# Performance work log

Hardware: AMD Instinct MI355X
Metric: run time of the kernel (lower is better)

## Reference

```python
import jax, jax.numpy as jnp
import numpy as np

D_MODEL = 768
NUM_HEADS = 12
D_HEAD = D_MODEL // NUM_HEADS


def setup_inputs() -> dict:
    key = jax.random.key(0)
    ks = jax.random.split(key, 11)
    B, S = 1, 4096
    s = 1.0 / np.sqrt(D_MODEL)
    inp = {
        'q': jax.random.normal(ks[0], (B, S, D_MODEL), dtype=jnp.float32),
        'k': jax.random.normal(ks[1], (B, S, D_MODEL), dtype=jnp.float32),
        'v': jax.random.normal(ks[2], (B, S, D_MODEL), dtype=jnp.float32),
        'wq': jax.random.normal(ks[3], (D_MODEL, D_MODEL), dtype=jnp.float32) * s,
        'bq': jnp.zeros((D_MODEL,), dtype=jnp.float32),
        'wk': jax.random.normal(ks[4], (D_MODEL, D_MODEL), dtype=jnp.float32) * s,
        'bk': jnp.zeros((D_MODEL,), dtype=jnp.float32),
        'wv': jax.random.normal(ks[5], (D_MODEL, D_MODEL), dtype=jnp.float32) * s,
        'bv': jnp.zeros((D_MODEL,), dtype=jnp.float32),
        'wo': jax.random.normal(ks[6], (D_MODEL, D_MODEL), dtype=jnp.float32) * s,
        'bo': jnp.zeros((D_MODEL,), dtype=jnp.float32),
    }
    return inp


def reference(q, k, v, wq, bq, wk, bk, wv, bv, wo, bo):
    B, S, _ = q.shape
    # linear projections (torch Linear: x @ W^T + b)
    qh = (q @ wq.T + bq).reshape(B, S, NUM_HEADS, D_HEAD).transpose(0, 2, 1, 3)
    kh = (k @ wk.T + bk).reshape(B, S, NUM_HEADS, D_HEAD).transpose(0, 2, 1, 3)
    vh = (v @ wv.T + bv).reshape(B, S, NUM_HEADS, D_HEAD).transpose(0, 2, 1, 3)
    scores = jnp.einsum('bhqd,bhkd->bhqk', qh, kh) / jnp.sqrt(jnp.float32(D_HEAD))
    causal = jnp.tril(jnp.ones((S, S), dtype=bool))  # [S,S] causal mask
    scores = jnp.where(causal, scores, jnp.finfo(scores.dtype).min)
    attn = jax.nn.softmax(scores, axis=-1)  # dropout omitted (eval mode)
    out = jnp.einsum('bhqk,bhkd->bhqd', attn, vh)
    out = out.transpose(0, 2, 1, 3).reshape(B, S, D_MODEL)
    return out @ wo.T + bo
```

## Files before the change

kernel.cpp:

```cpp
#include <hip/hip_runtime.h>
#include <stdint.h>

typedef __attribute__((ext_vector_type(8))) short short8;
typedef __attribute__((ext_vector_type(2))) float float2v;
typedef __attribute__((ext_vector_type(4))) float float4v;
typedef __attribute__((ext_vector_type(16))) float f32x16;
typedef __attribute__((ext_vector_type(2))) uint32_t uint32x2;
typedef __attribute__((ext_vector_type(4))) uint32_t uint32x4;
typedef __attribute__((ext_vector_type(2))) unsigned int uint2v;

__device__ __forceinline__ uint32_t pkbf(float a, float b) {
  uint32_t r;
  asm("v_cvt_pk_bf16_f32 %0, %1, %2" : "=v"(r) : "v"(a), "v"(b));
  return r;
}

__device__ __forceinline__ float2v pkadd(float2v a, float2v b) {
  float2v d;
  asm("v_pk_add_f32 %0, %1, %2" : "=v"(d) : "v"(a), "v"(b));
  return d;
}

__device__ __forceinline__ float fexp2(float x) {
#if __has_builtin(__builtin_amdgcn_exp2f)
  return __builtin_amdgcn_exp2f(x);
#else
  return exp2f(x);
#endif
}

__device__ __forceinline__ uint2v plswap(uint32_t a, uint32_t b) {
#if __has_builtin(__builtin_amdgcn_permlane32_swap)
  return __builtin_amdgcn_permlane32_swap(a, b, false, false);
#else
  asm("v_permlane32_swap_b32 %0, %1" : "+v"(a), "+v"(b));
  uint2v r;
  r[0] = a;
  r[1] = b;
  return r;
#endif
}

__device__ __forceinline__ void gll16(const unsigned short* g, unsigned short* l) {
  __builtin_amdgcn_global_load_lds(
      (const __attribute__((address_space(1))) void*)g,
      (__attribute__((address_space(3))) void*)l, 16, 0, 0);
}

struct CvtArgs {
  const float* src[7];
  unsigned short* dst[7];
};

__global__ __launch_bounds__(256) void cvt_all(CvtArgs a) {
  const int bid = blockIdx.x;
  int t, off;
  if (bid < 4608) { t = bid / 1536; off = bid - t * 1536; }
  else { const int b2 = bid - 4608; t = 3 + b2 / 288; off = b2 - (t - 3) * 288; }
  const size_t i = (size_t)off * 256 + threadIdx.x;
  const float4v* p = (const float4v*)(a.src[t] + i * 8);
  float4v x = p[0], y = p[1];
  uint32x4 o;
  o[0] = pkbf(x[0], x[1]);
  o[1] = pkbf(x[2], x[3]);
  o[2] = pkbf(y[0], y[1]);
  o[3] = pkbf(y[2], y[3]);
  *(uint32x4*)(a.dst[t] + i * 8) = o;
}

__global__ __launch_bounds__(256) void gemm_qkv(
    const unsigned short* __restrict__ xq, const unsigned short* __restrict__ xk,
    const unsigned short* __restrict__ xv,
    const unsigned short* __restrict__ wqb, const unsigned short* __restrict__ wkb,
    const unsigned short* __restrict__ wvb,
    const float* __restrict__ bq, const float* __restrict__ bk,
    const float* __restrict__ bv,
    unsigned short* __restrict__ Qp, unsigned short* __restrict__ Kp,
    unsigned short* __restrict__ Vt, float qscale)
{
  __shared__ unsigned short As[128 * 64];
  __shared__ unsigned short Ws[128 * 64];
  const int z = blockIdx.z;
  const unsigned short* A = z == 0 ? xq : z == 1 ? xk : xv;
  const unsigned short* W = z == 0 ? wqb : z == 1 ? wkb : wvb;
  const float* bias = z == 0 ? bq : z == 1 ? bk : bv;
  const int M = 4096, N = 768, K = 768;
  const int tid = threadIdx.x, wave = tid >> 6, lane = tid & 63;
  const int g = lane >> 4, l16 = lane & 15;
  const int sw = l16 & 7;
  const int m0 = blockIdx.x * 128, n0 = blockIdx.y * 128;
  const int wn = (wave >> 1) * 64, wm = (wave & 1) * 64;
  const int srow0 = wave * 32 + (lane >> 3);
  const int skg = lane & 7;

  float4v acc[4][4] = {};

  for (int k0 = 0; k0 < K; k0 += 64) {
    if (k0) __syncthreads();
    #pragma unroll
    for (int c = 0; c < 4; ++c) {
      const int row = srow0 + c * 8;
      const int kg = skg ^ (row & 7);
      gll16(A + (size_t)(m0 + row) * K + k0 + kg * 8, &As[(wave * 32 + c * 8) * 64]);
      gll16(W + (size_t)(n0 + row) * K + k0 + kg * 8, &Ws[(wave * 32 + c * 8) * 64]);
    }
    __syncthreads();
    #pragma unroll
    for (int kk = 0; kk < 2; ++kk) {
      const int kg = ((kk * 4 + g) ^ sw) * 8;
      short8 xf[4], wf[4];
      #pragma unroll
      for (int t = 0; t < 4; ++t) {
        xf[t] = *(const short8*)&As[(wm + t * 16 + l16) * 64 + kg];
        wf[t] = *(const short8*)&Ws[(wn + t * 16 + l16) * 64 + kg];
      }
      if (z < 2) {
        #pragma unroll
        for (int i = 0; i < 4; ++i)
          #pragma unroll
          for (int j = 0; j < 4; ++j)
            acc[i][j] = __builtin_amdgcn_mfma_f32_16x16x32_bf16(wf[i], xf[j], acc[i][j], 0, 0, 0);
      } else {
        #pragma unroll
        for (int i = 0; i < 4; ++i)
          #pragma unroll
          for (int j = 0; j < 4; ++j)
            acc[i][j] = __builtin_amdgcn_mfma_f32_16x16x32_bf16(xf[i], wf[j], acc[i][j], 0, 0, 0);
      }
    }
  }

  if (z < 2) {
    unsigned short* O = z == 0 ? Qp : Kp;
    const float osc = z == 0 ? qscale : 1.0f;
    #pragma unroll
    for (int i = 0; i < 4; ++i) {
      const int nb = n0 + wn + i * 16 + 4 * g;
      const float4v bb = *(const float4v*)&bias[nb];
      #pragma unroll
      for (int j = 0; j < 4; ++j) {
        const int m = m0 + wm + j * 16 + l16;
        uint32x2 pk;
        pk[0] = pkbf((acc[i][j][0] + bb[0]) * osc, (acc[i][j][1] + bb[1]) * osc);
        pk[1] = pkbf((acc[i][j][2] + bb[2]) * osc, (acc[i][j][3] + bb[3]) * osc);
        *(uint32x2*)(O + (size_t)m * N + nb) = pk;
      }
    }
  } else {
    #pragma unroll
    for (int j = 0; j < 4; ++j) {
      const int n = n0 + wn + j * 16 + l16;
      const float bb = bias[n];
      #pragma unroll
      for (int i = 0; i < 4; ++i) {
        const int mb = m0 + wm + i * 16 + 4 * g;
        uint32x2 pk;
        pk[0] = pkbf(acc[i][j][0] + bb, acc[i][j][1] + bb);
        pk[1] = pkbf(acc[i][j][2] + bb, acc[i][j][3] + bb);
        *(uint32x2*)(Vt + (size_t)n * M + mb) = pk;
      }
    }
  }
}

__global__ __launch_bounds__(256, 4) void flash_part(
    const unsigned short* __restrict__ Qp,
    const unsigned short* __restrict__ Kp,
    const unsigned short* __restrict__ Vt,
    unsigned short* __restrict__ Opart,
    float* __restrict__ lpart)
{
  __shared__ unsigned short lds_k[2][64 * 64];
  __shared__ unsigned short lds_v[2][64 * 64];
  const int S = 4096, DM = 768;

  const int gid = blockIdx.x;
  const int h = gid % 12;
  const int e = 79 - gid / 12;
  int t, c;
  if (e < 8)       { t = e;                c = 0; }
  else if (e < 24) { t = 8 + (e - 8) / 2;  c = (e - 8) % 2; }
  else if (e < 48) { t = 16 + (e - 24) / 3; c = (e - 24) % 3; }
  else             { t = 24 + (e - 48) / 4; c = (e - 48) % 4; }
  const int kb0 = c * 16;
  const int kbe = min(kb0 + 16, 2 * t + 2);

  const int tid = threadIdx.x, wave = tid >> 6, lane = tid & 63;
  const int l31 = lane & 31, hi = lane >> 5, sw7 = lane & 7;
  const int qbase = t * 128 + wave * 32;
  const int qrow = qbase + l31;

  short8 qf[4];
  {
    const unsigned short* qp = Qp + (size_t)qrow * DM + h * 64 + hi * 8;
    qf[0] = *(const short8*)(qp);
    qf[1] = *(const short8*)(qp + 16);
    qf[2] = *(const short8*)(qp + 32);
    qf[3] = *(const short8*)(qp + 48);
  }

  f32x16 o0 = {}, o1 = {};
  float2v lsA = {0.f, 0.f}, lsB = {0.f, 0.f};

  const int strow = wave * 16 + (lane >> 3);
  const int skg = lane & 7;

  #pragma unroll
  for (int cc = 0; cc < 2; ++cc) {
    const int row = strow + cc * 8;
    const int kg = skg ^ (row & 7);
    gll16(Kp + (size_t)(kb0 * 64 + row) * DM + h * 64 + kg * 8,
          &lds_k[0][(wave * 16 + cc * 8) * 64]);
    gll16(Vt + (size_t)(h * 64 + row) * S + kb0 * 64 + kg * 8,
          &lds_v[0][(wave * 16 + cc * 8) * 64]);
  }
  __syncthreads();

  for (int kb = kb0; kb < kbe; ++kb) {
    const int cur = kb & 1;
    if (kb + 1 < kbe) {
      const int nb = cur ^ 1;
      #pragma unroll
      for (int cc = 0; cc < 2; ++cc) {
        const int row = strow + cc * 8;
        const int kg = skg ^ (row & 7);
        gll16(Kp + (size_t)((kb + 1) * 64 + row) * DM + h * 64 + kg * 8,
              &lds_k[nb][(wave * 16 + cc * 8) * 64]);
        gll16(Vt + (size_t)(h * 64 + row) * S + (kb + 1) * 64 + kg * 8,
              &lds_v[nb][(wave * 16 + cc * 8) * 64]);
      }
    }
    const unsigned short* kc = lds_k[cur];
    const unsigned short* vc = lds_v[cur];

    f32x16 s0 = {}, s1 = {};
    __builtin_amdgcn_s_setprio(1);
    #pragma unroll
    for (int d4 = 0; d4 < 4; ++d4) {
      const int cg = ((2 * d4 + hi) ^ sw7) * 8;
      short8 ka = *(const short8*)&kc[l31 * 64 + cg];
      short8 kb2 = *(const short8*)&kc[(32 + l31) * 64 + cg];
      s0 = __builtin_amdgcn_mfma_f32_32x32x16_bf16(ka, qf[d4], s0, 0, 0, 0);
      s1 = __builtin_amdgcn_mfma_f32_32x32x16_bf16(kb2, qf[d4], s1, 0, 0, 0);
    }
    __builtin_amdgcn_s_setprio(0);

    const bool diag = (kb + 1) * 64 > qbase;
    short8 pb[4];
    auto sm_pack = [&](const f32x16& sv, int ks, short8* pbp) {
      #pragma unroll
      for (int jh = 0; jh < 2; ++jh) {
        float pe[8];
        if (diag) {
          #pragma unroll
          for (int rr = 0; rr < 8; ++rr) {
            const int key = kb * 64 + ks + (rr & 3) + 8 * (2 * jh + (rr >> 2)) + 4 * hi;
            pe[rr] = fexp2(key <= qrow ? sv[jh * 8 + rr] : -1e30f);
          }
        } else {
          #pragma unroll
          for (int rr = 0; rr < 8; ++rr) pe[rr] = fexp2(sv[jh * 8 + rr]);
        }
        float2v p01 = {pe[0], pe[1]}, p23 = {pe[2], pe[3]};
        float2v p45 = {pe[4], pe[5]}, p67 = {pe[6], pe[7]};
        lsA = pkadd(lsA, pkadd(p01, p45));
        lsB = pkadd(lsB, pkadd(p23, p67));
        const uint32_t x01 = pkbf(pe[0], pe[1]);
        const uint32_t x23 = pkbf(pe[2], pe[3]);
        const uint32_t y01 = pkbf(pe[4], pe[5]);
        const uint32_t y23 = pkbf(pe[6], pe[7]);
        uint2v r01 = plswap(x01, y01);
        uint2v r23 = plswap(x23, y23);
        union { uint32x4 u; short8 s; } w;
        w.u[0] = r01[0];
        w.u[1] = r23[0];
        w.u[2] = r01[1];
        w.u[3] = r23[1];
        pbp[jh] = w.s;
      }
    };
    sm_pack(s0, 0, &pb[0]);
    sm_pack(s1, 32, &pb[2]);

    __builtin_amdgcn_s_setprio(1);
    #pragma unroll
    for (int kk = 0; kk < 4; ++kk) {
      const int cg = ((2 * kk + hi) ^ sw7) * 8;
      short8 va0 = *(const short8*)&vc[l31 * 64 + cg];
      short8 va1 = *(const short8*)&vc[(32 + l31) * 64 + cg];
      o0 = __builtin_amdgcn_mfma_f32_32x32x16_bf16(va0, pb[kk], o0, 0, 0, 0);
      o1 = __builtin_amdgcn_mfma_f32_32x32x16_bf16(va1, pb[kk], o1, 0, 0, 0);
    }
    __builtin_amdgcn_s_setprio(0);

    __syncthreads();
  }

  float L = (lsA[0] + lsA[1]) + (lsB[0] + lsB[1]);
  L += __shfl_xor(L, 32);
  const int slot = (h * 32 + t) * 4 + c;
  if (hi == 0) lpart[slot * 128 + wave * 32 + l31] = L;
  unsigned short* ob = Opart + (size_t)slot * 8192 + (size_t)(wave * 32 + l31) * 64;
  #pragma unroll
  for (int dt = 0; dt < 2; ++dt) {
    const f32x16& oo = dt ? o1 : o0;
    #pragma unroll
    for (int a = 0; a < 4; ++a) {
      uint32x2 ov;
      ov[0] = pkbf(oo[4 * a + 0], oo[4 * a + 1]);
      ov[1] = pkbf(oo[4 * a + 2], oo[4 * a + 3]);
      *(uint32x2*)(ob + dt * 32 + 8 * a + 4 * hi) = ov;
    }
  }
}

__global__ __launch_bounds__(256) void flash_combine(
    const unsigned short* __restrict__ Opart, const float* __restrict__ lpart,
    unsigned short* __restrict__ AO)
{
  const int t = blockIdx.x, h = blockIdx.y;
  const int nc = (2 * t + 17) >> 4;
  const int slot0 = (h * 32 + t) * 4;
  const int tid = threadIdx.x;
  const int qr = tid >> 2, dc = (tid & 3) * 16;
  #pragma unroll
  for (int it = 0; it < 2; ++it) {
    const int ql = it * 64 + qr;
    float acc[16];
    #pragma unroll
    for (int j = 0; j < 16; ++j) acc[j] = 0.0f;
    float lsum = 0.0f;
    for (int cc = 0; cc < nc; ++cc) {
      const int slot = slot0 + cc;
      lsum += lpart[slot * 128 + ql];
      const uint32x4* p = (const uint32x4*)(Opart + (size_t)slot * 8192 + ql * 64 + dc);
      uint32x4 w0 = p[0], w1 = p[1];
      #pragma unroll
      for (int j = 0; j < 4; ++j) {
        union { uint32_t u; float f; } lo, hi;
        lo.u = w0[j] << 16; hi.u = w0[j] & 0xffff0000u;
        acc[2 * j] += lo.f; acc[2 * j + 1] += hi.f;
        lo.u = w1[j] << 16; hi.u = w1[j] & 0xffff0000u;
        acc[8 + 2 * j] += lo.f; acc[8 + 2 * j + 1] += hi.f;
      }
    }
    const float inv = 1.0f / lsum;
    uint32x4 o0, o1;
    #pragma unroll
    for (int j = 0; j < 4; ++j) {
      o0[j] = pkbf(acc[2 * j] * inv, acc[2 * j + 1] * inv);
      o1[j] = pkbf(acc[8 + 2 * j] * inv, acc[8 + 2 * j + 1] * inv);
    }
    unsigned short* dst = AO + (size_t)(t * 128 + ql) * 768 + h * 64 + dc;
    *(uint32x4*)dst = o0;
    *(uint32x4*)(dst + 8) = o1;
  }
}

__global__ __launch_bounds__(256) void gemm_out(
    const unsigned short* __restrict__ A, const unsigned short* __restrict__ W,
    const float* __restrict__ bias, float* __restrict__ Out)
{
  __shared__ unsigned short As[128 * 64];
  __shared__ unsigned short Ws[128 * 64];
  const int N = 768, K = 768;
  const int tid = threadIdx.x, wave = tid >> 6, lane = tid & 63;
  const int g = lane >> 4, l16 = lane & 15;
  const int sw = l16 & 7;
  const int m0 = blockIdx.x * 128, n0 = blockIdx.y * 128;
  const int wn = (wave >> 1) * 64, wm = (wave & 1) * 64;
  const int srow0 = wave * 32 + (lane >> 3);
  const int skg = lane & 7;

  float4v acc[4][4] = {};

  for (int k0 = 0; k0 < K; k0 += 64) {
    if (k0) __syncthreads();
    #pragma unroll
    for (int c = 0; c < 4; ++c) {
      const int row = srow0 + c * 8;
      const int kg = skg ^ (row & 7);
      gll16(A + (size_t)(m0 + row) * K + k0 + kg * 8, &As[(wave * 32 + c * 8) * 64]);
      gll16(W + (size_t)(n0 + row) * K + k0 + kg * 8, &Ws[(wave * 32 + c * 8) * 64]);
    }
    __syncthreads();
    #pragma unroll
    for (int kk = 0; kk < 2; ++kk) {
      const int kg = ((kk * 4 + g) ^ sw) * 8;
      short8 xf[4], wf[4];
      #pragma unroll
      for (int t = 0; t < 4; ++t) {
        xf[t] = *(const short8*)&As[(wm + t * 16 + l16) * 64 + kg];
        wf[t] = *(const short8*)&Ws[(wn + t * 16 + l16) * 64 + kg];
      }
      #pragma unroll
      for (int i = 0; i < 4; ++i)
        #pragma unroll
        for (int j = 0; j < 4; ++j)
          acc[i][j] = __builtin_amdgcn_mfma_f32_16x16x32_bf16(wf[i], xf[j], acc[i][j], 0, 0, 0);
    }
  }

  #pragma unroll
  for (int i = 0; i < 4; ++i) {
    const int nb = n0 + wn + i * 16 + 4 * g;
    const float4v bb = *(const float4v*)&bias[nb];
    #pragma unroll
    for (int j = 0; j < 4; ++j) {
      const int m = m0 + wm + j * 16 + l16;
      float4v ov;
      #pragma unroll
      for (int rr = 0; rr < 4; ++rr) ov[rr] = acc[i][j][rr] + bb[rr];
      *(float4v*)(Out + (size_t)m * N + nb) = ov;
    }
  }
}

extern "C" void kernel_launch(void* const* d_in, const int* in_sizes, int n_in,
                              void* d_out, int out_size, void* d_ws, size_t ws_size,
                              hipStream_t stream) {
  const float* q  = (const float*)d_in[0];
  const float* k  = (const float*)d_in[1];
  const float* v  = (const float*)d_in[2];
  const float* wq = (const float*)d_in[3];
  const float* bq = (const float*)d_in[4];
  const float* wk = (const float*)d_in[5];
  const float* bk = (const float*)d_in[6];
  const float* wv = (const float*)d_in[7];
  const float* bv = (const float*)d_in[8];
  const float* wo = (const float*)d_in[9];
  const float* bo = (const float*)d_in[10];
  float* out = (float*)d_out;

  const int S = 4096, D = 768;
  unsigned short* Qp    = (unsigned short*)d_ws;
  unsigned short* Kp    = Qp  + (size_t)S * D;
  unsigned short* Vt    = Kp  + (size_t)S * D;
  unsigned short* AO    = Vt  + (size_t)S * D;
  unsigned short* xq    = AO  + (size_t)S * D;
  unsigned short* xk    = xq  + (size_t)S * D;
  unsigned short* xv    = xk  + (size_t)S * D;
  unsigned short* wqb   = xv  + (size_t)S * D;
  unsigned short* wkb   = wqb + (size_t)D * D;
  unsigned short* wvb   = wkb + (size_t)D * D;
  unsigned short* wob   = wvb + (size_t)D * D;
  unsigned short* Opart = wob + (size_t)D * D;
  float*          lpart = (float*)(Opart + (size_t)1536 * 8192);

  CvtArgs ca;
  ca.src[0] = q;  ca.dst[0] = xq;
  ca.src[1] = k;  ca.dst[1] = xk;
  ca.src[2] = v;  ca.dst[2] = xv;
  ca.src[3] = wq; ca.dst[3] = wqb;
  ca.src[4] = wk; ca.dst[4] = wkb;
  ca.src[5] = wv; ca.dst[5] = wvb;
  ca.src[6] = wo; ca.dst[6] = wob;

  const float SC = 0.125f * 1.44269504089f;
  dim3 blk(256);
  cvt_all<<<dim3(5760), blk, 0, stream>>>(ca);
  gemm_qkv<<<dim3(32, 6, 3), blk, 0, stream>>>(xq, xk, xv, wqb, wkb, wvb,
                                               bq, bk, bv, Qp, Kp, Vt, SC);
  flash_part<<<dim3(960), blk, 0, stream>>>(Qp, Kp, Vt, Opart, lpart);
  flash_combine<<<dim3(32, 12), blk, 0, stream>>>(Opart, lpart, AO);
  gemm_out<<<dim3(32, 6), blk, 0, stream>>>(AO, wob, bo, out);
}
```

Before: 201.8 us.

## Double-buffer GEMM LDS tiles and widen flash key blocks to 128

After: 213.2 us. 5.7% more time.

```diff
diff --git a/kernel.cpp b/kernel.cpp
--- a/kernel.cpp
+++ b/kernel.cpp
@@ -78,8 +78,8 @@
     unsigned short* __restrict__ Qp, unsigned short* __restrict__ Kp,
     unsigned short* __restrict__ Vt, float qscale)
 {
-  __shared__ unsigned short As[128 * 64];
-  __shared__ unsigned short Ws[128 * 64];
+  __shared__ unsigned short As[2][128 * 64];
+  __shared__ unsigned short Ws[2][128 * 64];
   const int z = blockIdx.z;
   const unsigned short* A = z == 0 ? xq : z == 1 ? xk : xv;
   const unsigned short* W = z == 0 ? wqb : z == 1 ? wkb : wvb;
@@ -95,24 +95,30 @@
 
   float4v acc[4][4] = {};
 
-  for (int k0 = 0; k0 < K; k0 += 64) {
-    if (k0) __syncthreads();
+  auto stage = [&](int buf, int k0) {
     #pragma unroll
     for (int c = 0; c < 4; ++c) {
       const int row = srow0 + c * 8;
       const int kg = skg ^ (row & 7);
-      gll16(A + (size_t)(m0 + row) * K + k0 + kg * 8, &As[(wave * 32 + c * 8) * 64]);
-      gll16(W + (size_t)(n0 + row) * K + k0 + kg * 8, &Ws[(wave * 32 + c * 8) * 64]);
-    }
-    __syncthreads();
+      gll16(A + (size_t)(m0 + row) * K + k0 + kg * 8, &As[buf][(wave * 32 + c * 8) * 64]);
+      gll16(W + (size_t)(n0 + row) * K + k0 + kg * 8, &Ws[buf][(wave * 32 + c * 8) * 64]);
+    }
+  };
+
+  stage(0, 0);
+  __syncthreads();
+
+  for (int k0 = 0; k0 < K; k0 += 64) {
+    const int cur = (k0 >> 6) & 1;
+    if (k0 + 64 < K) stage(cur ^ 1, k0 + 64);
     #pragma unroll
     for (int kk = 0; kk < 2; ++kk) {
       const int kg = ((kk * 4 + g) ^ sw) * 8;
       short8 xf[4], wf[4];
       #pragma unroll
       for (int t = 0; t < 4; ++t) {
-        xf[t] = *(const short8*)&As[(wm + t * 16 + l16) * 64 + kg];
-        wf[t] = *(const short8*)&Ws[(wn + t * 16 + l16) * 64 + kg];
+        xf[t] = *(const short8*)&As[cur][(wm + t * 16 + l16) * 64 + kg];
+        wf[t] = *(const short8*)&Ws[cur][(wn + t * 16 + l16) * 64 + kg];
       }
       if (z < 2) {
         #pragma unroll
@@ -128,6 +134,7 @@
             acc[i][j] = __builtin_amdgcn_mfma_f32_16x16x32_bf16(xf[i], wf[j], acc[i][j], 0, 0, 0);
       }
     }
+    __syncthreads();
   }
 
   if (z < 2) {
@@ -163,27 +170,27 @@
   }
 }
 
-__global__ __launch_bounds__(256, 4) void flash_part(
+__global__ __launch_bounds__(256, 2) void flash_part(
     const unsigned short* __restrict__ Qp,
     const unsigned short* __restrict__ Kp,
     const unsigned short* __restrict__ Vt,
     unsigned short* __restrict__ Opart,
     float* __restrict__ lpart)
 {
-  __shared__ unsigned short lds_k[2][64 * 64];
-  __shared__ unsigned short lds_v[2][64 * 64];
+  __shared__ unsigned short lds_k[2][128 * 64];
+  __shared__ unsigned short lds_v[2][128 * 64];
   const int S = 4096, DM = 768;
 
   const int gid = blockIdx.x;
   const int h = gid % 12;
   const int e = 79 - gid / 12;
   int t, c;
-  if (e < 8)       { t = e;                c = 0; }
-  else if (e < 24) { t = 8 + (e - 8) / 2;  c = (e - 8) % 2; }
+  if (e < 8)       { t = e;                 c = 0; }
+  else if (e < 24) { t = 8 + (e - 8) / 2;   c = (e - 8) % 2; }
   else if (e < 48) { t = 16 + (e - 24) / 3; c = (e - 24) % 3; }
   else             { t = 24 + (e - 48) / 4; c = (e - 48) % 4; }
-  const int kb0 = c * 16;
-  const int kbe = min(kb0 + 16, 2 * t + 2);
+  const int kb0 = c * 8;
+  const int kbe = min(kb0 + 8, t + 1);
 
   const int tid = threadIdx.x, wave = tid >> 6, lane = tid & 63;
   const int l31 = lane & 31, hi = lane >> 5, sw7 = lane & 7;
@@ -202,59 +209,40 @@
   f32x16 o0 = {}, o1 = {};
   float2v lsA = {0.f, 0.f}, lsB = {0.f, 0.f};
 
-  const int strow = wave * 16 + (lane >> 3);
   const int skg = lane & 7;
 
-  #pragma unroll
-  for (int cc = 0; cc < 2; ++cc) {
-    const int row = strow + cc * 8;
-    const int kg = skg ^ (row & 7);
-    gll16(Kp + (size_t)(kb0 * 64 + row) * DM + h * 64 + kg * 8,
-          &lds_k[0][(wave * 16 + cc * 8) * 64]);
-    gll16(Vt + (size_t)(h * 64 + row) * S + kb0 * 64 + kg * 8,
-          &lds_v[0][(wave * 16 + cc * 8) * 64]);
-  }
+  auto stage = [&](int buf, int kb) {
+    #pragma unroll
+    for (int cc = 0; cc < 4; ++cc) {
+      const int ln = wave * 32 + cc * 8 + (lane >> 3);
+      const int kgk = skg ^ (ln & 7);
+      gll16(Kp + (size_t)(kb * 128 + ln) * DM + h * 64 + kgk * 8,
+            &lds_k[buf][(wave * 32 + cc * 8) * 64]);
+      const int swv = ((ln >> 1) ^ ((ln & 1) << 2)) & 7;
+      const int kgv = skg ^ swv;
+      gll16(Vt + (size_t)(h * 64 + (ln >> 1)) * S + kb * 128 + (ln & 1) * 64 + kgv * 8,
+            &lds_v[buf][(wave * 32 + cc * 8) * 64]);
+    }
+  };
+
+  stage(0, kb0);
   __syncthreads();
 
   for (int kb = kb0; kb < kbe; ++kb) {
-    const int cur = kb & 1;
-    if (kb + 1 < kbe) {
-      const int nb = cur ^ 1;
-      #pragma unroll
-      for (int cc = 0; cc < 2; ++cc) {
-        const int row = strow + cc * 8;
-        const int kg = skg ^ (row & 7);
-        gll16(Kp + (size_t)((kb + 1) * 64 + row) * DM + h * 64 + kg * 8,
-              &lds_k[nb][(wave * 16 + cc * 8) * 64]);
-        gll16(Vt + (size_t)(h * 64 + row) * S + (kb + 1) * 64 + kg * 8,
-              &lds_v[nb][(wave * 16 + cc * 8) * 64]);
-      }
-    }
+    const int cur = (kb - kb0) & 1;
+    if (kb + 1 < kbe) stage(cur ^ 1, kb + 1);
     const unsigned short* kc = lds_k[cur];
     const unsigned short* vc = lds_v[cur];
 
-    f32x16 s0 = {}, s1 = {};
-    __builtin_amdgcn_s_setprio(1);
-    #pragma unroll
-    for (int d4 = 0; d4 < 4; ++d4) {
-      const int cg = ((2 * d4 + hi) ^ sw7) * 8;
-      short8 ka = *(const short8*)&kc[l31 * 64 + cg];
-      short8 kb2 = *(const short8*)&kc[(32 + l31) * 64 + cg];
-      s0 = __builtin_amdgcn_mfma_f32_32x32x16_bf16(ka, qf[d4], s0, 0, 0, 0);
-      s1 = __builtin_amdgcn_mfma_f32_32x32x16_bf16(kb2, qf[d4], s1, 0, 0, 0);
-    }
-    __builtin_amdgcn_s_setprio(0);
-
-    const bool diag = (kb + 1) * 64 > qbase;
-    short8 pb[4];
-    auto sm_pack = [&](const f32x16& sv, int ks, short8* pbp) {
+    short8 pbA[4], pbB[4];
+    auto sm_pack = [&](const f32x16& sv, int ks, bool diag, short8* pbp) {
       #pragma unroll
       for (int jh = 0; jh < 2; ++jh) {
         float pe[8];
         if (diag) {
           #pragma unroll
           for (int rr = 0; rr < 8; ++rr) {
-            const int key = kb * 64 + ks + (rr & 3) + 8 * (2 * jh + (rr >> 2)) + 4 * hi;
+            const int key = kb * 128 + ks + (rr & 3) + 8 * (2 * jh + (rr >> 2)) + 4 * hi;
             pe[rr] = fexp2(key <= qrow ? sv[jh * 8 + rr] : -1e30f);
           }
         } else {
@@ -279,17 +267,57 @@
         pbp[jh] = w.s;
       }
     };
-    sm_pack(s0, 0, &pb[0]);
-    sm_pack(s1, 32, &pb[2]);
-
+
+    const bool diagA = (kb * 128 + 64) > qbase;
+    const bool diagB = (kb * 128 + 128) > qbase;
+
+    f32x16 s0 = {}, s1 = {};
     __builtin_amdgcn_s_setprio(1);
+    #pragma unroll
+    for (int d4 = 0; d4 < 4; ++d4) {
+      const int cg = ((2 * d4 + hi) ^ sw7) * 8;
+      short8 ka = *(const short8*)&kc[l31 * 64 + cg];
+      short8 kb2 = *(const short8*)&kc[(32 + l31) * 64 + cg];
+      s0 = __builtin_amdgcn_mfma_f32_32x32x16_bf16(ka, qf[d4], s0, 0, 0, 0);
+      s1 = __builtin_amdgcn_mfma_f32_32x32x16_bf16(kb2, qf[d4], s1, 0, 0, 0);
+    }
+    __builtin_amdgcn_s_setprio(0);
+
+    sm_pack(s0, 0, diagA, &pbA[0]);
+    sm_pack(s1, 32, diagA, &pbA[2]);
+
+    f32x16 s2 = {}, s3 = {};
+    __builtin_amdgcn_s_setprio(1);
+    #pragma unroll
+    for (int d4 = 0; d4 < 4; ++d4) {
+      const int cg = ((2 * d4 + hi) ^ sw7) * 8;
+      short8 ka = *(const short8*)&kc[(64 + l31) * 64 + cg];
+      short8 kb2 = *(const short8*)&kc[(96 + l31) * 64 + cg];
+      s2 = __builtin_amdgcn_mfma_f32_32x32x16_bf16(ka, qf[d4], s2, 0, 0, 0);
+      s3 = __builtin_amdgcn_mfma_f32_32x32x16_bf16(kb2, qf[d4], s3, 0, 0, 0);
+    }
+
     #pragma unroll
     for (int kk = 0; kk < 4; ++kk) {
       const int cg = ((2 * kk + hi) ^ sw7) * 8;
-      short8 va0 = *(const short8*)&vc[l31 * 64 + cg];
-      short8 va1 = *(const short8*)&vc[(32 + l31) * 64 + cg];
-      o0 = __builtin_amdgcn_mfma_f32_32x32x16_bf16(va0, pb[kk], o0, 0, 0, 0);
-      o1 = __builtin_amdgcn_mfma_f32_32x32x16_bf16(va1, pb[kk], o1, 0, 0, 0);
+      short8 va0 = *(const short8*)&vc[(2 * l31) * 64 + cg];
+      short8 va1 = *(const short8*)&vc[(64 + 2 * l31) * 64 + cg];
+      o0 = __builtin_amdgcn_mfma_f32_32x32x16_bf16(va0, pbA[kk], o0, 0, 0, 0);
+      o1 = __builtin_amdgcn_mfma_f32_32x32x16_bf16(va1, pbA[kk], o1, 0, 0, 0);
+    }
+    __builtin_amdgcn_s_setprio(0);
+
+    sm_pack(s2, 64, diagB, &pbB[0]);
+    sm_pack(s3, 96, diagB, &pbB[2]);
+
+    __builtin_amdgcn_s_setprio(1);
+    #pragma unroll
+    for (int kk = 0; kk < 4; ++kk) {
+      const int cg = ((2 * kk + hi) ^ sw7 ^ 4) * 8;
+      short8 va0 = *(const short8*)&vc[(2 * l31 + 1) * 64 + cg];
+      short8 va1 = *(const short8*)&vc[(64 + 2 * l31 + 1) * 64 + cg];
+      o0 = __builtin_amdgcn_mfma_f32_32x32x16_bf16(va0, pbB[kk], o0, 0, 0, 0);
+      o1 = __builtin_amdgcn_mfma_f32_32x32x16_bf16(va1, pbB[kk], o1, 0, 0, 0);
     }
     __builtin_amdgcn_s_setprio(0);
 
@@ -319,7 +347,7 @@
     unsigned short* __restrict__ AO)
 {
   const int t = blockIdx.x, h = blockIdx.y;
-  const int nc = (2 * t + 17) >> 4;
+  const int nc = (t + 8) >> 3;
   const int slot0 = (h * 32 + t) * 4;
   const int tid = threadIdx.x;
   const int qr = tid >> 2, dc = (tid & 3) * 16;
@@ -361,8 +389,8 @@
     const unsigned short* __restrict__ A, const unsigned short* __restrict__ W,
     const float* __restrict__ bias, float* __restrict__ Out)
 {
-  __shared__ unsigned short As[128 * 64];
-  __shared__ unsigned short Ws[128 * 64];
+  __shared__ unsigned short As[2][128 * 64];
+  __shared__ unsigned short Ws[2][128 * 64];
   const int N = 768, K = 768;
   const int tid = threadIdx.x, wave = tid >> 6, lane = tid & 63;
   const int g = lane >> 4, l16 = lane & 15;
@@ -374,24 +402,30 @@
 
   float4v acc[4][4] = {};
 
-  for (int k0 = 0; k0 < K; k0 += 64) {
-    if (k0) __syncthreads();
+  auto stage = [&](int buf, int k0) {
     #pragma unroll
     for (int c = 0; c < 4; ++c) {
       const int row = srow0 + c * 8;
       const int kg = skg ^ (row & 7);
-      gll16(A + (size_t)(m0 + row) * K + k0 + kg * 8, &As[(wave * 32 + c * 8) * 64]);
-      gll16(W + (size_t)(n0 + row) * K + k0 + kg * 8, &Ws[(wave * 32 + c * 8) * 64]);
-    }
-    __syncthreads();
+      gll16(A + (size_t)(m0 + row) * K + k0 + kg * 8, &As[buf][(wave * 32 + c * 8) * 64]);
+      gll16(W + (size_t)(n0 + row) * K + k0 + kg * 8, &Ws[buf][(wave * 32 + c * 8) * 64]);
+    }
+  };
+
+  stage(0, 0);
+  __syncthreads();
+
+  for (int k0 = 0; k0 < K; k0 += 64) {
+    const int cur = (k0 >> 6) & 1;
+    if (k0 + 64 < K) stage(cur ^ 1, k0 + 64);
     #pragma unroll
     for (int kk = 0; kk < 2; ++kk) {
       const int kg = ((kk * 4 + g) ^ sw) * 8;
       short8 xf[4], wf[4];
       #pragma unroll
       for (int t = 0; t < 4; ++t) {
-        xf[t] = *(const short8*)&As[(wm + t * 16 + l16) * 64 + kg];
-        wf[t] = *(const short8*)&Ws[(wn + t * 16 + l16) * 64 + kg];
+        xf[t] = *(const short8*)&As[cur][(wm + t * 16 + l16) * 64 + kg];
+        wf[t] = *(const short8*)&Ws[cur][(wn + t * 16 + l16) * 64 + kg];
       }
       #pragma unroll
       for (int i = 0; i < 4; ++i)
@@ -399,6 +433,7 @@
         for (int j = 0; j < 4; ++j)
           acc[i][j] = __builtin_amdgcn_mfma_f32_16x16x32_bf16(wf[i], xf[j], acc[i][j], 0, 0, 0);
     }
+    __syncthreads();
   }
 
   #pragma unroll
```
